# Performance work log

Hardware: AMD Instinct MI355X
Metric: run time of the kernel (lower is better)

Reference implementation:

```python
import jax, jax.numpy as jnp
import numpy as np

B, S, D_MODEL, K_CH, OUT = 16, 8192, 256, 256, 256


def setup_inputs() -> dict:
    key = jax.random.key(0)
    ks = jax.random.split(key, 9)
    s = lambda fan_in: 1.0 / np.sqrt(fan_in)
    return {
        "query": jax.random.normal(ks[0], (B, D_MODEL), dtype=jnp.float32),
        "key": jax.random.normal(ks[1], (B, S, K_CH), dtype=jnp.float32),
        "value": jax.random.normal(ks[2], (B, S, K_CH), dtype=jnp.float32),
        "Wq": jax.random.uniform(ks[3], (D_MODEL, OUT), jnp.float32, -s(D_MODEL), s(D_MODEL)),
        "bq": jax.random.uniform(ks[4], (OUT,), jnp.float32, -s(D_MODEL), s(D_MODEL)),
        "Wk": jax.random.uniform(ks[5], (K_CH, OUT), jnp.float32, -s(K_CH), s(K_CH)),
        "bk": jax.random.uniform(ks[6], (OUT,), jnp.float32, -s(K_CH), s(K_CH)),
        "Wv": jax.random.uniform(ks[7], (K_CH, OUT), jnp.float32, -s(K_CH), s(K_CH)),
        "bv": jax.random.uniform(ks[8], (OUT,), jnp.float32, -s(K_CH), s(K_CH)),
    }


def reference(query, key, value, Wq, bq, Wk, bk, Wv, bv):
    # q is a single vector per batch; the torch module expands it to S identical
    # rows, making every output row identical. We compute one row and broadcast
    # -- mathematically identical, O(S*d) instead of O(S^2*d).
    q = query @ Wq + bq                      # [B, OUT]
    k = jnp.einsum("bsc,co->bso", key, Wk) + bk    # [B, S, OUT]
    v = jnp.einsum("bsc,co->bso", value, Wv) + bv  # [B, S, OUT]
    scale = 1.0 / jnp.sqrt(jnp.float32(q.shape[-1]))
    scores = jnp.einsum("bo,bso->bs", q, k) * scale  # [B, S]
    w = jax.nn.softmax(scores, axis=-1)              # [B, S]
    ctx = jnp.einsum("bs,bso->bo", w, v)             # [B, OUT]
    seq_len = k.shape[1]
    return jnp.broadcast_to(ctx[:, None, :], (ctx.shape[0], seq_len, ctx.shape[1]))
```

## Files before the change

kernel.cpp:

```cpp
#include <hip/hip_runtime.h>

typedef float f4 __attribute__((ext_vector_type(4)));

constexpr int Bn = 16;
constexpr int Sn = 8192;
constexpr int Dn = 256;
constexpr float kScale = 0.0625f;
constexpr int NCHUNK = 128;
constexpr int CHUNK  = Sn / NCHUNK;
constexpr int OROWS  = 128;

constexpr int R_OFF    = 0;
constexpr int C_OFF    = R_OFF + Bn * Dn;
constexpr int M_OFF    = C_OFF + 64;
constexpr int SUM_OFF  = M_OFF + Bn * NCHUNK;
constexpr int PART_OFF = SUM_OFF + Bn * NCHUNK;

__global__ __launch_bounds__(256) void k_qrc(
    const float* __restrict__ query, const float* __restrict__ Wq,
    const float* __restrict__ bq, const float* __restrict__ Wk,
    const float* __restrict__ bk, float* __restrict__ ws) {
  int b = blockIdx.x, t = threadIdx.x;
  __shared__ float qs[Dn];
  __shared__ float qh[Dn];
  __shared__ float red[256];
  qs[t] = query[b * Dn + t];
  __syncthreads();
  float acc = bq[t];
  #pragma unroll 32
  for (int d = 0; d < Dn; ++d) acc += qs[d] * Wq[d * Dn + t];
  qh[t] = acc;
  __syncthreads();
  float racc = 0.f;
  const f4* wkrow = (const f4*)(Wk + (size_t)t * Dn);
  const f4* qh4 = (const f4*)qh;
  #pragma unroll 16
  for (int o4 = 0; o4 < Dn / 4; ++o4) {
    f4 wv = wkrow[o4];
    f4 qv = qh4[o4];
    racc += wv.x * qv.x + wv.y * qv.y + wv.z * qv.z + wv.w * qv.w;
  }
  ws[R_OFF + b * Dn + t] = racc;
  red[t] = qh[t] * bk[t];
  __syncthreads();
  for (int off = 128; off; off >>= 1) {
    if (t < off) red[t] += red[t + off];
    __syncthreads();
  }
  if (t == 0) ws[C_OFF + b] = red[0];
}

__global__ __launch_bounds__(256) void k_fused(
    const float* __restrict__ key, const float* __restrict__ value,
    float* __restrict__ ws) {
  int blk = blockIdx.x;
  int b = blk >> 7;
  int chunk = blk & 127;
  int s0 = chunk * CHUNK;
  int t = threadIdx.x, lane = t & 63, wv = t >> 6;

  __shared__ float wm[4], wsum[4];
  __shared__ f4 wva[4][64];

  f4 rv = ((const f4*)(ws + R_OFF + b * Dn))[lane];
  float cb = ws[C_OFF + b];
  const f4* kp = (const f4*)(key + ((size_t)b * Sn + s0) * Dn);
  const f4* vp = (const f4*)(value + ((size_t)b * Sn + s0) * Dn);

  float m = -1e30f, sum = 0.f;
  f4 vacc = {0.f, 0.f, 0.f, 0.f};

  #pragma unroll 4
  for (int i = 0; i < CHUNK / 4; ++i) {
    int sl = wv + 4 * i;
    f4 kv = __builtin_nontemporal_load(&kp[(size_t)sl * 64 + lane]);
    f4 vv = __builtin_nontemporal_load(&vp[(size_t)sl * 64 + lane]);
    float dot = kv.x * rv.x + kv.y * rv.y + kv.z * rv.z + kv.w * rv.w;
    #pragma unroll
    for (int off = 32; off; off >>= 1) dot += __shfl_xor(dot, off, 64);
    float s = (dot + cb) * kScale;
    if (s > m) {
      float sc = __expf(m - s);
      sum *= sc;
      vacc *= sc;
      m = s;
    }
    float w = __expf(s - m);
    sum += w;
    vacc += w * vv;
  }

  if (lane == 0) { wm[wv] = m; wsum[wv] = sum; }
  wva[wv][lane] = vacc;
  __syncthreads();

  float gm = fmaxf(fmaxf(wm[0], wm[1]), fmaxf(wm[2], wm[3]));
  float e0 = __expf(wm[0] - gm), e1 = __expf(wm[1] - gm);
  float e2 = __expf(wm[2] - gm), e3 = __expf(wm[3] - gm);
  const float* v0 = (const float*)&wva[0][0];
  const float* v1 = (const float*)&wva[1][0];
  const float* v2 = (const float*)&wva[2][0];
  const float* v3 = (const float*)&wva[3][0];
  float part = v0[t] * e0 + v1[t] * e1 + v2[t] * e2 + v3[t] * e3;
  ws[PART_OFF + ((size_t)b * NCHUNK + chunk) * Dn + t] = part;
  if (t == 0) {
    ws[M_OFF + b * NCHUNK + chunk] = gm;
    ws[SUM_OFF + b * NCHUNK + chunk] =
        wsum[0] * e0 + wsum[1] * e1 + wsum[2] * e2 + wsum[3] * e3;
  }
}

__global__ __launch_bounds__(256) void k_out(
    const float* __restrict__ Wv, const float* __restrict__ bv,
    const float* __restrict__ ws, float* __restrict__ out) {
  int blk = blockIdx.x;
  int b = blk >> 6;
  int oc = blk & 63;
  int s0 = oc * OROWS;
  int t = threadIdx.x, lane = t & 63, wv = t >> 6;

  __shared__ float msh[NCHUNK];
  __shared__ float ssh[NCHUNK];
  __shared__ float e[NCHUNK];
  __shared__ float ush[Dn];
  __shared__ float ctx[Dn];

  if (t < NCHUNK) msh[t] = ws[M_OFF + b * NCHUNK + t];
  else            ssh[t - NCHUNK] = ws[SUM_OFF + b * NCHUNK + (t - NCHUNK)];
  __syncthreads();
  float gm = -1e30f;
  #pragma unroll 16
  for (int c = 0; c < NCHUNK; ++c) gm = fmaxf(gm, msh[c]);
  if (t < NCHUNK) e[t] = __expf(msh[t] - gm);
  __syncthreads();
  float denom = 0.f;
  #pragma unroll 16
  for (int c = 0; c < NCHUNK; ++c) denom += ssh[c] * e[c];
  float u = 0.f;
  #pragma unroll 16
  for (int c = 0; c < NCHUNK; ++c)
    u += ws[PART_OFF + ((size_t)b * NCHUNK + c) * Dn + t] * e[c];
  ush[t] = u / denom;
  __syncthreads();
  float acc = bv[t];
  #pragma unroll 16
  for (int o = 0; o < Dn; ++o) acc += ush[o] * Wv[o * Dn + t];
  ctx[t] = acc;
  __syncthreads();

  f4 val = ((const f4*)ctx)[lane];
  f4* op = (f4*)(out + ((size_t)b * Sn + s0) * Dn);
  #pragma unroll 8
  for (int it = 0; it < OROWS / 4; ++it) {
    int sl = wv + 4 * it;
    __builtin_nontemporal_store(val, &op[(size_t)sl * 64 + lane]);
  }
}

extern "C" void kernel_launch(void* const* d_in, const int* in_sizes, int n_in,
                              void* d_out, int out_size, void* d_ws, size_t ws_size,
                              hipStream_t stream) {
  const float* query = (const float*)d_in[0];
  const float* key   = (const float*)d_in[1];
  const float* value = (const float*)d_in[2];
  const float* Wq    = (const float*)d_in[3];
  const float* bq    = (const float*)d_in[4];
  const float* Wk    = (const float*)d_in[5];
  const float* bk    = (const float*)d_in[6];
  const float* Wv    = (const float*)d_in[7];
  const float* bv    = (const float*)d_in[8];
  float* out = (float*)d_out;
  float* ws  = (float*)d_ws;

  hipLaunchKernelGGL(k_qrc,   dim3(Bn),          dim3(256), 0, stream,
                     query, Wq, bq, Wk, bk, ws);
  hipLaunchKernelGGL(k_fused, dim3(Bn * NCHUNK), dim3(256), 0, stream,
                     key, value, ws);
  hipLaunchKernelGGL(k_out,   dim3(Bn * 64),     dim3(256), 0, stream,
                     Wv, bv, ws, out);
}
```

Before: 100.2 us.

## Software-pipeline key/value loads and batch four rows per online-softmax step

Restructures the per-chunk streaming loop so each wave owns a contiguous 16-row block and processes four rows per step. Loads for the next group are issued before the current group is reduced, which acts as a register double buffer. The four dot-product reductions are interleaved, and the running max is rescaled once per group instead of once per row. The scale factor is also folded into rv and cb ahead of the loop. The cost is higher register pressure and dropping the nontemporal load hints, which may change cache behaviour on a purely streaming read.

```diff
diff --git a/kernel.cpp b/kernel.cpp
--- a/kernel.cpp
+++ b/kernel.cpp
@@ -62,32 +62,70 @@
   __shared__ float wm[4], wsum[4];
   __shared__ f4 wva[4][64];
 
-  f4 rv = ((const f4*)(ws + R_OFF + b * Dn))[lane];
-  float cb = ws[C_OFF + b];
+  f4 rv = ((const f4*)(ws + R_OFF + b * Dn))[lane] * kScale;
+  float cb = ws[C_OFF + b] * kScale;
   const f4* kp = (const f4*)(key + ((size_t)b * Sn + s0) * Dn);
   const f4* vp = (const f4*)(value + ((size_t)b * Sn + s0) * Dn);
 
   float m = -1e30f, sum = 0.f;
   f4 vacc = {0.f, 0.f, 0.f, 0.f};
-
-  #pragma unroll 4
-  for (int i = 0; i < CHUNK / 4; ++i) {
-    int sl = wv + 4 * i;
-    f4 kv = __builtin_nontemporal_load(&kp[(size_t)sl * 64 + lane]);
-    f4 vv = __builtin_nontemporal_load(&vp[(size_t)sl * 64 + lane]);
-    float dot = kv.x * rv.x + kv.y * rv.y + kv.z * rv.z + kv.w * rv.w;
+  int rbase = wv * 16;
+
+  f4 kv0, kv1, kv2, kv3, vv0, vv1, vv2, vv3;
+  kv0 = kp[(size_t)(rbase + 0) * 64 + lane];
+  kv1 = kp[(size_t)(rbase + 1) * 64 + lane];
+  kv2 = kp[(size_t)(rbase + 2) * 64 + lane];
+  kv3 = kp[(size_t)(rbase + 3) * 64 + lane];
+  vv0 = vp[(size_t)(rbase + 0) * 64 + lane];
+  vv1 = vp[(size_t)(rbase + 1) * 64 + lane];
+  vv2 = vp[(size_t)(rbase + 2) * 64 + lane];
+  vv3 = vp[(size_t)(rbase + 3) * 64 + lane];
+
+  #pragma unroll
+  for (int g = 0; g < 4; ++g) {
+    f4 kn0, kn1, kn2, kn3, vn0, vn1, vn2, vn3;
+    if (g < 3) {
+      int rn = rbase + (g + 1) * 4;
+      kn0 = kp[(size_t)(rn + 0) * 64 + lane];
+      kn1 = kp[(size_t)(rn + 1) * 64 + lane];
+      kn2 = kp[(size_t)(rn + 2) * 64 + lane];
+      kn3 = kp[(size_t)(rn + 3) * 64 + lane];
+      vn0 = vp[(size_t)(rn + 0) * 64 + lane];
+      vn1 = vp[(size_t)(rn + 1) * 64 + lane];
+      vn2 = vp[(size_t)(rn + 2) * 64 + lane];
+      vn3 = vp[(size_t)(rn + 3) * 64 + lane];
+    }
+    f4 d;
+    d.x = kv0.x * rv.x + kv0.y * rv.y + kv0.z * rv.z + kv0.w * rv.w;
+    d.y = kv1.x * rv.x + kv1.y * rv.y + kv1.z * rv.z + kv1.w * rv.w;
+    d.z = kv2.x * rv.x + kv2.y * rv.y + kv2.z * rv.z + kv2.w * rv.w;
+    d.w = kv3.x * rv.x + kv3.y * rv.y + kv3.z * rv.z + kv3.w * rv.w;
     #pragma unroll
-    for (int off = 32; off; off >>= 1) dot += __shfl_xor(dot, off, 64);
-    float s = (dot + cb) * kScale;
-    if (s > m) {
-      float sc = __expf(m - s);
+    for (int off = 32; off; off >>= 1) {
+      f4 o;
+      o.x = __shfl_xor(d.x, off, 64);
+      o.y = __shfl_xor(d.y, off, 64);
+      o.z = __shfl_xor(d.z, off, 64);
+      o.w = __shfl_xor(d.w, off, 64);
+      d += o;
+    }
+    f4 s = d + cb;
+    float sg = fmaxf(fmaxf(s.x, s.y), fmaxf(s.z, s.w));
+    if (sg > m) {
+      float sc = __expf(m - sg);
       sum *= sc;
       vacc *= sc;
-      m = s;
+      m = sg;
     }
-    float w = __expf(s - m);
-    sum += w;
-    vacc += w * vv;
+    float w0 = __expf(s.x - m), w1 = __expf(s.y - m);
+    float w2 = __expf(s.z - m), w3 = __expf(s.w - m);
+    sum += (w0 + w1) + (w2 + w3);
+    vacc += w0 * vv0;
+    vacc += w1 * vv1;
+    vacc += w2 * vv2;
+    vacc += w3 * vv3;
+    kv0 = kn0; kv1 = kn1; kv2 = kn2; kv3 = kn3;
+    vv0 = vn0; vv1 = vn1; vv2 = vn2; vv3 = vn3;
   }
 
   if (lane == 0) { wm[wv] = m; wsum[wv] = sum; }
```

Measured after the change: 98.36 us. About the same (-1.8%).
